# Kernel tuning notes

Measured on AMD Instinct MI355X. Metric: run time of the kernel, lower is better.

The kernel has to match this reference:

```python
import jax, jax.numpy as jnp
import numpy as np

L, S, N, E, H = 1024, 1024, 4, 1024, 16


def setup_inputs() -> dict:
    key = jax.random.key(0)
    ks = jax.random.split(key, 7)
    return {
        "query": jax.random.normal(ks[0], (L, N, E), jnp.float32),
        "key": jax.random.normal(ks[1], (S, N, E), jnp.float32),
        "value": jax.random.normal(ks[2], (S, N, E), jnp.float32),
        "in_proj_weight": jax.random.normal(ks[3], (3 * E, E), jnp.float32) * (E ** -0.5),
        "in_proj_bias": jax.random.normal(ks[4], (3 * E,), jnp.float32) * 0.02,
        "out_proj_weight": jax.random.normal(ks[5], (E, E), jnp.float32) * (E ** -0.5),
        "out_proj_bias": jax.random.normal(ks[6], (E,), jnp.float32) * 0.02,
        "num_heads": H,
    }


def _split_heads(x, n, h, hd):
    # (T, N, E) -> (N*h, T, hd), matching torch view(T, N*h, hd).transpose(0, 1)
    t = x.shape[0]
    return jnp.transpose(x.reshape(t, n * h, hd), (1, 0, 2))


def reference(query, key, value, in_proj_weight, in_proj_bias,
              out_proj_weight, out_proj_bias, num_heads):
    tgt_len, bsz, embed_dim = query.shape
    src_len = key.shape[0]
    head_dim = embed_dim // num_heads
    scaling = float(head_dim) ** -0.5

    # packed QKV projection (torch F.linear: x @ W.T + b), sliced as in source
    q = query @ in_proj_weight[:embed_dim].T + in_proj_bias[:embed_dim]
    k = key @ in_proj_weight[embed_dim:2 * embed_dim].T + in_proj_bias[embed_dim:2 * embed_dim]
    v = value @ in_proj_weight[2 * embed_dim:].T + in_proj_bias[2 * embed_dim:]
    q = q * scaling

    q = _split_heads(q, bsz, num_heads, head_dim)  # (N*H, L, hd)
    k = _split_heads(k, bsz, num_heads, head_dim)  # (N*H, S, hd)
    v = _split_heads(v, bsz, num_heads, head_dim)  # (N*H, S, hd)

    scores = jnp.einsum('bld,bsd->bls', q, k)           # (N*H, L, S)
    attn = jax.nn.softmax(scores, axis=-1)
    ctx = jnp.einsum('bls,bsd->bld', attn, v)           # (N*H, L, hd)

    # (N*H, L, hd) -> (L, N, E)
    ctx = jnp.transpose(ctx, (1, 0, 2)).reshape(tgt_len, bsz, embed_dim)
    attn_output = ctx @ out_proj_weight.T + out_proj_bias

    # need_weights=True path: average over heads -> (N, L, S)
    attn_weights = attn.reshape(bsz, num_heads, tgt_len, src_len).sum(axis=1) / num_heads
    return attn_output, attn_weights
```

## Files before the change

### kernel.cpp

```cpp
#include <hip/hip_runtime.h>

typedef unsigned short u16;
typedef __attribute__((ext_vector_type(8))) short short8;
typedef __attribute__((ext_vector_type(4))) float f32x4;

__device__ __forceinline__ u16 f2bf(float f) {
  unsigned int i = __float_as_uint(f);
  i += 0x7fffu + ((i >> 16) & 1u);
  return (u16)(i >> 16);
}

__device__ __forceinline__ short8 cvt8(const float* p) {
  float4 a = ((const float4*)p)[0];
  float4 b = ((const float4*)p)[1];
  short8 r;
  r[0] = (short)f2bf(a.x); r[1] = (short)f2bf(a.y);
  r[2] = (short)f2bf(a.z); r[3] = (short)f2bf(a.w);
  r[4] = (short)f2bf(b.x); r[5] = (short)f2bf(b.y);
  r[6] = (short)f2bf(b.z); r[7] = (short)f2bf(b.w);
  return r;
}

__global__ __launch_bounds__(256) void convert_bf16(
    const float* __restrict__ q, const float* __restrict__ k,
    const float* __restrict__ v, const float* __restrict__ Wi,
    const float* __restrict__ Wo,
    u16* __restrict__ qb, u16* __restrict__ kb, u16* __restrict__ vb,
    u16* __restrict__ Wib, u16* __restrict__ Wob)
{
  const float* src; u16* dst; int len8;
  switch (blockIdx.y) {
    case 0:  src = q;  dst = qb;  len8 = 524288; break;
    case 1:  src = k;  dst = kb;  len8 = 524288; break;
    case 2:  src = v;  dst = vb;  len8 = 524288; break;
    case 3:  src = Wi; dst = Wib; len8 = 393216; break;
    default: src = Wo; dst = Wob; len8 = 131072; break;
  }
  int stride = gridDim.x * 256;
  for (int i = blockIdx.x * 256 + threadIdx.x; i < len8; i += stride)
    *(short8*)(dst + (size_t)i * 8) = cvt8(src + (size_t)i * 8);
}

__global__ __launch_bounds__(256) void qkv_gemm(
    const u16* __restrict__ qb, const u16* __restrict__ kb,
    const u16* __restrict__ vb, const u16* __restrict__ W,
    const float* __restrict__ bias,
    u16* __restrict__ qh, u16* __restrict__ kh, u16* __restrict__ vt)
{
  __shared__ __align__(16) u16 SH[16384];

  const int tid  = threadIdx.x;
  const int wave = tid >> 6;
  const int lane = tid & 63;
  const int r    = lane & 15;
  const int q4   = lane >> 4;
  const int wm   = wave >> 1;
  const int wn   = wave & 1;

  const int orig = blockIdx.y * 24 + blockIdx.x;
  const int nid  = (orig & 7) * 96 + (orig >> 3);
  const int mt   = nid / 24;
  const int jt   = nid - mt * 24;
  const int src  = jt >> 3;
  const u16* X = (src == 0) ? qb : (src == 1) ? kb : vb;
  const int m0 = mt * 128;
  const int j0 = jt * 128;

  const int lrow = lane >> 2;
  const int lchk = ((lane & 3) ^ ((lane >> 3) & 3)) << 4;
  const char* Xc = (const char*)X;
  const char* Wc = (const char*)W;

  const int fchk = (q4 ^ ((r >> 1) & 3)) << 3;

  f32x4 acc[4][4];
  #pragma unroll
  for (int a = 0; a < 4; ++a)
    #pragma unroll
    for (int b = 0; b < 4; ++b)
      acc[a][b] = (f32x4){0.f, 0.f, 0.f, 0.f};

  auto STAGE = [&](int buf, int kt) {
    const int kbyte = kt * 64;
    u16* Ad = SH + buf * 4096;
    u16* Bd = SH + 8192 + buf * 4096;
    #pragma unroll
    for (int i = 0; i < 2; ++i) {
      const int g = wave * 2 + i;
      __builtin_amdgcn_global_load_lds(
          (const u16*)(Xc + (size_t)(m0 + g * 16 + lrow) * 2048 + kbyte + lchk),
          Ad + g * 512, 16, 0, 0);
      __builtin_amdgcn_global_load_lds(
          (const u16*)(Wc + (size_t)(j0 + g * 16 + lrow) * 2048 + kbyte + lchk),
          Bd + g * 512, 16, 0, 0);
    }
  };

  STAGE(0, 0);
  for (int kt = 0; kt < 32; ++kt) {
    const int cur = kt & 1;
    __syncthreads();
    if (kt < 31) STAGE(cur ^ 1, kt + 1);

    const u16* As = SH + cur * 4096;
    const u16* Bs = SH + 8192 + cur * 4096;
    short8 af[4], bf[4];
    #pragma unroll
    for (int mi = 0; mi < 4; ++mi)
      af[mi] = *(const short8*)(&As[(wm * 64 + mi * 16 + r) * 32 + fchk]);
    #pragma unroll
    for (int ji = 0; ji < 4; ++ji)
      bf[ji] = *(const short8*)(&Bs[(wn * 64 + ji * 16 + r) * 32 + fchk]);
    #pragma unroll
    for (int mi = 0; mi < 4; ++mi)
      #pragma unroll
      for (int ji = 0; ji < 4; ++ji)
        acc[mi][ji] = __builtin_amdgcn_mfma_f32_16x16x32_bf16(af[mi], bf[ji], acc[mi][ji], 0, 0, 0);
  }

  __syncthreads();
  const int h0 = (j0 & 1023) >> 6;
  const int t0 = mt * 32;
  if (src < 2) {
    #pragma unroll
    for (int mi = 0; mi < 4; ++mi) {
      const int tt = wm * 16 + mi * 4 + q4;
      #pragma unroll
      for (int ji = 0; ji < 4; ++ji) {
        const int jj = wn * 64 + ji * 16 + r;
        const int dd = jj & 63, hq = jj >> 6;
        const int cs = (((dd >> 3) ^ (tt & 7)) << 3) + (dd & 7);
        #pragma unroll
        for (int rr = 0; rr < 4; ++rr) {
          float v = acc[mi][ji][rr] + bias[j0 + jj];
          SH[((rr * 2 + hq) * 32 + tt) * 64 + cs] =
              (src == 0) ? f2bf(v * 0.125f) : f2bf(v);
        }
      }
    }
    __syncthreads();
    u16* dst = (src == 0) ? qh : kh;
    #pragma unroll
    for (int c = 0; c < 8; ++c) {
      const int cid = c * 256 + tid;
      const int nn = cid >> 9, hq = (cid >> 8) & 1, tt = (cid >> 3) & 31, dc = cid & 7;
      short8 vv = *(const short8*)(SH + ((nn * 2 + hq) * 32 + tt) * 64 +
                                   ((dc ^ (tt & 7)) << 3));
      *(short8*)(dst + (size_t)(nn * 16 + h0 + hq) * 65536 +
                 (size_t)(t0 + tt) * 64 + dc * 8) = vv;
    }
  } else {
    #pragma unroll
    for (int mi = 0; mi < 4; ++mi) {
      const int tt = wm * 16 + mi * 4 + q4;
      const int tc = tt >> 3, toff = tt & 7;
      #pragma unroll
      for (int ji = 0; ji < 4; ++ji) {
        const int jj = wn * 64 + ji * 16 + r;
        const int dd = jj & 63, hq = jj >> 6;
        #pragma unroll
        for (int rr = 0; rr < 4; ++rr) {
          float v = acc[mi][ji][rr] + bias[j0 + jj];
          SH[((rr * 2 + hq) * 64 + dd) * 32 + ((tc ^ (dd & 3)) << 3) + toff] = f2bf(v);
        }
      }
    }
    __syncthreads();
    #pragma unroll
    for (int c = 0; c < 8; ++c) {
      const int cid = c * 256 + tid;
      const int bbv = cid >> 8, dd = (cid >> 2) & 63, tc = cid & 3;
      short8 vv = *(const short8*)(SH + (bbv * 64 + dd) * 32 +
                                   ((tc ^ (dd & 3)) << 3));
      const int bb = (bbv >> 1) * 16 + h0 + (bbv & 1);
      *(short8*)(vt + (size_t)bb * 65536 + (size_t)dd * 1024 + t0 + tc * 8) = vv;
    }
  }
}

__global__ __launch_bounds__(256) void attn_ctx_mfma(
    const u16* __restrict__ qh, const u16* __restrict__ kh,
    const u16* __restrict__ vt, u16* __restrict__ ctx,
    float* __restrict__ Zbuf)
{
  __shared__ __align__(16) u16 Ks[2][4096];
  __shared__ __align__(16) u16 Vs[2][4096];
  __shared__ __align__(16) u16 Pl[4][1024];

  const int tid = threadIdx.x;
  const int wv = tid >> 6, lane = tid & 63, r = lane & 15, q4 = lane >> 4;
  const int b  = blockIdx.y;
  const int lw = blockIdx.x * 64 + wv * 16;
  const int n = b >> 4, h = b & 15;

  const u16* qbase = qh + (size_t)b * 65536;
  const char* kc = (const char*)(kh + (size_t)b * 65536);
  const char* vc = (const char*)(vt + (size_t)b * 65536);
  u16* P = Pl[wv];

  const int ls  = lane >> 3;
  const int swzb = ((lane & 7) ^ ls) << 4;
  const int iw  = wv * 2;
  const size_t klo = (size_t)iw * 1024 + (size_t)ls * 128 + swzb;
  const size_t vlo = (size_t)iw * 16384 + (size_t)ls * 2048 + swzb;

  const int rsw = r & 7;
  const int c0 = (q4 ^ rsw) << 3;
  const int c1 = ((q4 ^ rsw) ^ 4) << 3;

  short8 aq0 = *(const short8*)(qbase + (size_t)(lw + r) * 64 + q4 * 8);
  short8 aq1 = *(const short8*)(qbase + (size_t)(lw + r) * 64 + 32 + q4 * 8);

  f32x4 oc[4];
  #pragma unroll
  for (int ji = 0; ji < 4; ++ji) oc[ji] = (f32x4){0.f, 0.f, 0.f, 0.f};
  float z[4] = {0.f, 0.f, 0.f, 0.f};

  {
    const char* kp = kc + klo;
    const char* vp = vc + vlo;
    u16* kd = &Ks[0][iw * 512];
    u16* vd = &Vs[0][iw * 512];
    __builtin_amdgcn_global_load_lds(kp,          kd,       16, 0, 0);
    __builtin_amdgcn_global_load_lds(kp + 1024,   kd + 512, 16, 0, 0);
    __builtin_amdgcn_global_load_lds(vp,          vd,       16, 0, 0);
    __builtin_amdgcn_global_load_lds(vp + 16384,  vd + 512, 16, 0, 0);
  }

  for (int it = 0; it < 16; ++it) {
    const int cur = it & 1;
    __syncthreads();
    const u16* Kb = Ks[cur];
    const u16* Vb = Vs[cur];

    f32x4 sc[4];
    #pragma unroll
    for (int ji = 0; ji < 4; ++ji) {
      const int row = (ji * 16 + r) * 64;
      short8 bk0 = *(const short8*)(Kb + row + c0);
      short8 bk1 = *(const short8*)(Kb + row + c1);
      f32x4 t = (f32x4){0.f, 0.f, 0.f, 0.f};
      t = __builtin_amdgcn_mfma_f32_16x16x32_bf16(aq0, bk0, t, 0, 0, 0);
      t = __builtin_amdgcn_mfma_f32_16x16x32_bf16(aq1, bk1, t, 0, 0, 0);
      sc[ji] = t;
    }

    if (it < 15) {
      const char* kp = kc + (size_t)(it + 1) * 8192 + klo;
      const char* vp = vc + (size_t)(it + 1) * 128  + vlo;
      u16* kd = &Ks[cur ^ 1][iw * 512];
      u16* vd = &Vs[cur ^ 1][iw * 512];
      __builtin_amdgcn_global_load_lds(kp,          kd,       16, 0, 0);
      __builtin_amdgcn_global_load_lds(kp + 1024,   kd + 512, 16, 0, 0);
      __builtin_amdgcn_global_load_lds(vp,          vd,       16, 0, 0);
      __builtin_amdgcn_global_load_lds(vp + 16384,  vd + 512, 16, 0, 0);
    }

    #pragma unroll
    for (int ji = 0; ji < 4; ++ji) {
      const int cw = ji * 2 + (r >> 3);
      #pragma unroll
      for (int rr = 0; rr < 4; ++rr) {
        float e = __expf(sc[ji][rr]);
        z[rr] += e;
        const int row = q4 * 4 + rr;
        P[row * 64 + ((cw ^ (row & 7)) << 3) + (r & 7)] = f2bf(e);
      }
    }
    asm volatile("s_waitcnt lgkmcnt(0)" ::: "memory");
    short8 ap0 = *(const short8*)(P + r * 64 + c0);
    short8 ap1 = *(const short8*)(P + r * 64 + c1);
    #pragma unroll
    for (int ji = 0; ji < 4; ++ji) {
      const int row = (ji * 16 + r) * 64;
      short8 bv0 = *(const short8*)(Vb + row + c0);
      short8 bv1 = *(const short8*)(Vb + row + c1);
      oc[ji] = __builtin_amdgcn_mfma_f32_16x16x32_bf16(ap0, bv0, oc[ji], 0, 0, 0);
      oc[ji] = __builtin_amdgcn_mfma_f32_16x16x32_bf16(ap1, bv1, oc[ji], 0, 0, 0);
    }
  }

  #pragma unroll
  for (int rr = 0; rr < 4; ++rr) {
    float zz = z[rr];
    zz += __shfl_xor(zz, 1);
    zz += __shfl_xor(zz, 2);
    zz += __shfl_xor(zz, 4);
    zz += __shfl_xor(zz, 8);
    z[rr] = zz;
  }

  #pragma unroll
  for (int rr = 0; rr < 4; ++rr) {
    float inv = 1.0f / z[rr];
    int l = lw + q4 * 4 + rr;
    u16* crow = ctx + ((size_t)l * 4 + n) * 1024 + h * 64;
    #pragma unroll
    for (int ji = 0; ji < 4; ++ji)
      crow[ji * 16 + r] = f2bf(oc[ji][rr] * inv);
    if (r == 0) Zbuf[(size_t)b * 1024 + l] = z[rr];
  }
}

__global__ __launch_bounds__(256) void attn_w_mfma(
    const u16* __restrict__ qh, const u16* __restrict__ kh,
    const float* __restrict__ Zbuf, float* __restrict__ out_w)
{
  __shared__ __align__(16) u16 Kw[2][4096];
  __shared__ float invZ[16][64];

  const int tid = threadIdx.x;
  const int wv = tid >> 6, lane = tid & 63, r = lane & 15, q4 = lane >> 4;
  const int lt = blockIdx.x;
  const int st = blockIdx.y;
  const int n  = blockIdx.z;
  const int l0 = lt * 64;
  const int s0 = st * 64;
  const int lw = l0 + wv * 16;

  const char* khc = (const char*)kh + (size_t)n * 2097152;

  const int ls  = lane >> 3;
  const int swzb = ((lane & 7) ^ ls) << 4;
  const int iw  = wv * 2;
  const size_t klo = (size_t)s0 * 128 + (size_t)iw * 1024 + (size_t)ls * 128 + swzb;

  const int rsw = r & 7;
  const int c0 = (q4 ^ rsw) << 3;
  const int c1 = ((q4 ^ rsw) ^ 4) << 3;

  for (int i = tid; i < 1024; i += 256) {
    int hh = i >> 6, row = i & 63;
    invZ[hh][row] = 1.0f / (Zbuf[(size_t)(n * 16 + hh) * 1024 + l0 + row] * 16.0f);
  }

  {
    const char* kp = khc + klo;
    u16* kd = &Kw[0][iw * 512];
    __builtin_amdgcn_global_load_lds(kp,        kd,       16, 0, 0);
    __builtin_amdgcn_global_load_lds(kp + 1024, kd + 512, 16, 0, 0);
  }
  const u16* q0 = qh + (size_t)(n * 16) * 65536;
  short8 aqc0 = *(const short8*)(q0 + (size_t)(lw + r) * 64 + q4 * 8);
  short8 aqc1 = *(const short8*)(q0 + (size_t)(lw + r) * 64 + 32 + q4 * 8);

  f32x4 wacc[4];
  #pragma unroll
  for (int ji = 0; ji < 4; ++ji) wacc[ji] = (f32x4){0.f, 0.f, 0.f, 0.f};

  for (int hh = 0; hh < 16; ++hh) {
    const int cur = hh & 1;
    __syncthreads();
    if (hh < 15) {
      const char* kp = khc + (size_t)(hh + 1) * 131072 + klo;
      u16* kd = &Kw[cur ^ 1][iw * 512];
      __builtin_amdgcn_global_load_lds(kp,        kd,       16, 0, 0);
      __builtin_amdgcn_global_load_lds(kp + 1024, kd + 512, 16, 0, 0);
    }
    const int hn = (hh < 15) ? hh + 1 : hh;
    const u16* qn = qh + (size_t)(n * 16 + hn) * 65536;
    short8 an0 = *(const short8*)(qn + (size_t)(lw + r) * 64 + q4 * 8);
    short8 an1 = *(const short8*)(qn + (size_t)(lw + r) * 64 + 32 + q4 * 8);

    const u16* Kb = Kw[cur];
    f32x4 sc[4];
    #pragma unroll
    for (int ji = 0; ji < 4; ++ji) {
      const int row = (ji * 16 + r) * 64;
      short8 bk0 = *(const short8*)(Kb + row + c0);
      short8 bk1 = *(const short8*)(Kb + row + c1);
      f32x4 t = (f32x4){0.f, 0.f, 0.f, 0.f};
      t = __builtin_amdgcn_mfma_f32_16x16x32_bf16(aqc0, bk0, t, 0, 0, 0);
      t = __builtin_amdgcn_mfma_f32_16x16x32_bf16(aqc1, bk1, t, 0, 0, 0);
      sc[ji] = t;
    }
    #pragma unroll
    for (int rr = 0; rr < 4; ++rr) {
      float iv = invZ[hh][wv * 16 + q4 * 4 + rr];
      #pragma unroll
      for (int ji = 0; ji < 4; ++ji)
        wacc[ji][rr] += __expf(sc[ji][rr]) * iv;
    }
    aqc0 = an0; aqc1 = an1;
  }

  #pragma unroll
  for (int ji = 0; ji < 4; ++ji)
    #pragma unroll
    for (int rr = 0; rr < 4; ++rr) {
      int row = lw + q4 * 4 + rr;
      int col = s0 + ji * 16 + r;
      out_w[(size_t)n * 1048576 + (size_t)row * 1024 + col] = wacc[ji][rr];
    }
}

__global__ __launch_bounds__(256) void out_gemm(
    const u16* __restrict__ ctx, const u16* __restrict__ W,
    const float* __restrict__ bias, float* __restrict__ out)
{
  __shared__ __align__(16) u16 As[2][128 * 32];
  __shared__ __align__(16) u16 Bs[2][64 * 32];

  const int tid  = threadIdx.x;
  const int wave = tid >> 6;
  const int lane = tid & 63;
  const int r    = lane & 15;
  const int q4   = lane >> 4;
  const int wm   = wave >> 1;
  const int wn   = wave & 1;

  const int orig = blockIdx.y * 16 + blockIdx.x;
  const int nid  = (orig & 7) * 64 + (orig >> 3);
  const int mt   = nid >> 4;
  const int jt   = nid & 15;
  const int m0 = mt * 128;
  const int j0 = jt * 64;

  const int lrow = lane >> 2;
  const int lchk = ((lane & 3) ^ ((lane >> 3) & 3)) << 4;
  const char* Ac = (const char*)ctx;
  const char* Wc = (const char*)W;
  const int fchk = (q4 ^ ((r >> 1) & 3)) << 3;

  f32x4 acc[4][2];
  #pragma unroll
  for (int a = 0; a < 4; ++a)
    #pragma unroll
    for (int b = 0; b < 2; ++b)
      acc[a][b] = (f32x4){0.f, 0.f, 0.f, 0.f};

  auto STAGE = [&](int buf, int kt) {
    const int kbyte = kt * 64;
    #pragma unroll
    for (int i = 0; i < 2; ++i) {
      const int g = wave * 2 + i;
      __builtin_amdgcn_global_load_lds(
          (const u16*)(Ac + (size_t)(m0 + g * 16 + lrow) * 2048 + kbyte + lchk),
          &As[buf][g * 512], 16, 0, 0);
    }
    __builtin_amdgcn_global_load_lds(
        (const u16*)(Wc + (size_t)(j0 + wave * 16 + lrow) * 2048 + kbyte + lchk),
        &Bs[buf][wave * 512], 16, 0, 0);
  };

  STAGE(0, 0);
  for (int kt = 0; kt < 32; ++kt) {
    const int cur = kt & 1;
    __syncthreads();
    if (kt < 31) STAGE(cur ^ 1, kt + 1);

    short8 af[4], bf[2];
    #pragma unroll
    for (int mi = 0; mi < 4; ++mi)
      af[mi] = *(const short8*)(&As[cur][(wm * 64 + mi * 16 + r) * 32 + fchk]);
    #pragma unroll
    for (int ji = 0; ji < 2; ++ji)
      bf[ji] = *(const short8*)(&Bs[cur][(wn * 32 + ji * 16 + r) * 32 + fchk]);
    #pragma unroll
    for (int mi = 0; mi < 4; ++mi)
      #pragma unroll
      for (int ji = 0; ji < 2; ++ji)
        acc[mi][ji] = __builtin_amdgcn_mfma_f32_16x16x32_bf16(af[mi], bf[ji], acc[mi][ji], 0, 0, 0);
  }

  #pragma unroll
  for (int mi = 0; mi < 4; ++mi) {
    #pragma unroll
    for (int ji = 0; ji < 2; ++ji) {
      #pragma unroll
      for (int rr = 0; rr < 4; ++rr) {
        int m = m0 + wm * 64 + mi * 16 + q4 * 4 + rr;
        int j = j0 + wn * 32 + ji * 16 + r;
        out[(size_t)m * 1024 + j] = acc[mi][ji][rr] + bias[j];
      }
    }
  }
}

extern "C" void kernel_launch(void* const* d_in, const int* in_sizes, int n_in,
                              void* d_out, int out_size, void* d_ws, size_t ws_size,
                              hipStream_t stream) {
  const float* query = (const float*)d_in[0];
  const float* key   = (const float*)d_in[1];
  const float* value = (const float*)d_in[2];
  const float* W_in  = (const float*)d_in[3];
  const float* b_in  = (const float*)d_in[4];
  const float* W_out = (const float*)d_in[5];
  const float* b_out = (const float*)d_in[6];
  float* out = (float*)d_out;

  u16* qb  = (u16*)d_ws;
  u16* kb  = qb  + (size_t)4194304;
  u16* vb  = kb  + (size_t)4194304;
  u16* Wib = vb  + (size_t)4194304;
  u16* Wob = Wib + (size_t)3145728;
  u16* qh  = Wob + (size_t)1048576;
  u16* kh  = qh  + (size_t)4194304;
  u16* vt  = kh  + (size_t)4194304;
  u16* ctx = vt  + (size_t)4194304;
  float* Zbuf = (float*)(ctx + (size_t)4194304);

  convert_bf16<<<dim3(512, 5), 256, 0, stream>>>(query, key, value, W_in, W_out,
                                                 qb, kb, vb, Wib, Wob);
  qkv_gemm<<<dim3(24, 32), 256, 0, stream>>>(qb, kb, vb, Wib, b_in, qh, kh, vt);
  attn_ctx_mfma<<<dim3(16, 64), 256, 0, stream>>>(qh, kh, vt, ctx, Zbuf);
  attn_w_mfma<<<dim3(16, 16, 4), 256, 0, stream>>>(qh, kh, Zbuf, out + (size_t)4194304);
  out_gemm<<<dim3(16, 32), 256, 0, stream>>>(ctx, Wob, b_out, out);
}
```

Measured before the change: 245.8 us.

## Triple-buffer LDS staging in QKV and output GEMMs with explicit vmcnt waits

Both projection GEMMs move from a double-buffered LDS pipeline to a three-stage ring, prefetching two k-tiles ahead. The __syncthreads is replaced by an inline s_waitcnt vmcnt(N) plus s_barrier, so only the oldest tile's async global->LDS loads must finish before compute. This hides more global-load latency at the cost of extra LDS per block (48KB for qkv_gemm), which may reduce occupancy. It also depends on correct hand-written waitcnt values.

```diff
diff --git a/kernel.cpp b/kernel.cpp
--- a/kernel.cpp
+++ b/kernel.cpp
@@ -47,7 +47,7 @@
     const float* __restrict__ bias,
     u16* __restrict__ qh, u16* __restrict__ kh, u16* __restrict__ vt)
 {
-  __shared__ __align__(16) u16 SH[16384];
+  __shared__ __align__(16) u16 SH[24576];
 
   const int tid  = threadIdx.x;
   const int wave = tid >> 6;
@@ -83,7 +83,7 @@
   auto STAGE = [&](int buf, int kt) {
     const int kbyte = kt * 64;
     u16* Ad = SH + buf * 4096;
-    u16* Bd = SH + 8192 + buf * 4096;
+    u16* Bd = SH + 12288 + buf * 4096;
     #pragma unroll
     for (int i = 0; i < 2; ++i) {
       const int g = wave * 2 + i;
@@ -96,14 +96,9 @@
     }
   };
 
-  STAGE(0, 0);
-  for (int kt = 0; kt < 32; ++kt) {
-    const int cur = kt & 1;
-    __syncthreads();
-    if (kt < 31) STAGE(cur ^ 1, kt + 1);
-
-    const u16* As = SH + cur * 4096;
-    const u16* Bs = SH + 8192 + cur * 4096;
+  auto COMPUTE = [&](int cb) {
+    const u16* As = SH + cb * 4096;
+    const u16* Bs = SH + 12288 + cb * 4096;
     short8 af[4], bf[4];
     #pragma unroll
     for (int mi = 0; mi < 4; ++mi)
@@ -116,7 +111,22 @@
       #pragma unroll
       for (int ji = 0; ji < 4; ++ji)
         acc[mi][ji] = __builtin_amdgcn_mfma_f32_16x16x32_bf16(af[mi], bf[ji], acc[mi][ji], 0, 0, 0);
-  }
+  };
+
+  STAGE(0, 0);
+  STAGE(1, 1);
+  int cb = 0;
+  for (int kt = 0; kt < 31; ++kt) {
+    asm volatile("s_waitcnt vmcnt(4) lgkmcnt(0)\n\ts_barrier" ::: "memory");
+    if (kt < 30) {
+      int nb = cb + 2; if (nb >= 3) nb -= 3;
+      STAGE(nb, kt + 2);
+    }
+    COMPUTE(cb);
+    if (++cb == 3) cb = 0;
+  }
+  asm volatile("s_waitcnt vmcnt(0) lgkmcnt(0)\n\ts_barrier" ::: "memory");
+  COMPUTE(cb);
 
   __syncthreads();
   const int h0 = (j0 & 1023) >> 6;
@@ -398,8 +408,7 @@
     const u16* __restrict__ ctx, const u16* __restrict__ W,
     const float* __restrict__ bias, float* __restrict__ out)
 {
-  __shared__ __align__(16) u16 As[2][128 * 32];
-  __shared__ __align__(16) u16 Bs[2][64 * 32];
+  __shared__ __align__(16) u16 SH[18432];
 
   const int tid  = threadIdx.x;
   const int wave = tid >> 6;
@@ -431,37 +440,51 @@
 
   auto STAGE = [&](int buf, int kt) {
     const int kbyte = kt * 64;
+    u16* Ad = SH + buf * 4096;
+    u16* Bd = SH + 12288 + buf * 2048;
     #pragma unroll
     for (int i = 0; i < 2; ++i) {
       const int g = wave * 2 + i;
       __builtin_amdgcn_global_load_lds(
           (const u16*)(Ac + (size_t)(m0 + g * 16 + lrow) * 2048 + kbyte + lchk),
-          &As[buf][g * 512], 16, 0, 0);
+          Ad + g * 512, 16, 0, 0);
     }
     __builtin_amdgcn_global_load_lds(
         (const u16*)(Wc + (size_t)(j0 + wave * 16 + lrow) * 2048 + kbyte + lchk),
-        &Bs[buf][wave * 512], 16, 0, 0);
+        Bd + wave * 512, 16, 0, 0);
   };
 
-  STAGE(0, 0);
-  for (int kt = 0; kt < 32; ++kt) {
-    const int cur = kt & 1;
-    __syncthreads();
-    if (kt < 31) STAGE(cur ^ 1, kt + 1);
-
+  auto COMPUTE = [&](int cb) {
+    const u16* As = SH + cb * 4096;
+    const u16* Bs = SH + 12288 + cb * 2048;
     short8 af[4], bf[2];
     #pragma unroll
     for (int mi = 0; mi < 4; ++mi)
-      af[mi] = *(const short8*)(&As[cur][(wm * 64 + mi * 16 + r) * 32 + fchk]);
+      af[mi] = *(const short8*)(&As[(wm * 64 + mi * 16 + r) * 32 + fchk]);
     #pragma unroll
     for (int ji = 0; ji < 2; ++ji)
-      bf[ji] = *(const short8*)(&Bs[cur][(wn * 32 + ji * 16 + r) * 32 + fchk]);
+      bf[ji] = *(const short8*)(&Bs[(wn * 32 + ji * 16 + r) * 32 + fchk]);
     #pragma unroll
     for (int mi = 0; mi < 4; ++mi)
       #pragma unroll
       for (int ji = 0; ji < 2; ++ji)
         acc[mi][ji] = __builtin_amdgcn_mfma_f32_16x16x32_bf16(af[mi], bf[ji], acc[mi][ji], 0, 0, 0);
-  }
+  };
+
+  STAGE(0, 0);
+  STAGE(1, 1);
+  int cb = 0;
+  for (int kt = 0; kt < 31; ++kt) {
+    asm volatile("s_waitcnt vmcnt(3) lgkmcnt(0)\n\ts_barrier" ::: "memory");
+    if (kt < 30) {
+      int nb = cb + 2; if (nb >= 3) nb -= 3;
+      STAGE(nb, kt + 2);
+    }
+    COMPUTE(cb);
+    if (++cb == 3) cb = 0;
+  }
+  asm volatile("s_waitcnt vmcnt(0) lgkmcnt(0)\n\ts_barrier" ::: "memory");
+  COMPUTE(cb);
 
   #pragma unroll
   for (int mi = 0; mi < 4; ++mi) {
```

After: 232.4 us. -5.5%, faster.
